# Optimization experiments

Measured on AMD Instinct MI355X. Metric: run time of the kernel, lower is better.

Reference implementation:

```python
import jax, jax.numpy as jnp
import numpy as np

B, N, NC = 16, 25200, 80          # batch, raw predictions, classes (COCO)
CONF_THRES = 0.25
IOU_THRES = 0.45
MAX_CAND = 1000                    # candidates kept after score top-k (pre-NMS)
CLS_OFFSET = 4096.0                # class-wise box offset (non-agnostic NMS trick)
EPS = 1e-7


def setup_inputs() -> dict:
    key = jax.random.key(0)
    # raw head output: [x, y, w, h, obj, cls0..cls79], values in [0,1]
    pred = jax.random.uniform(key, (B, N, 5 + NC), dtype=jnp.float32)
    return {"pred": pred}


def _xywh2xyxy(x):
    xy, wh = x[..., :2], x[..., 2:4]
    return jnp.concatenate([xy - wh * 0.5, xy + wh * 0.5], axis=-1)


def _box_iou(boxes):
    # boxes: [C, 4] xyxy -> pairwise IoU [C, C]
    area = (boxes[:, 2] - boxes[:, 0]) * (boxes[:, 3] - boxes[:, 1])
    lt = jnp.maximum(boxes[:, None, :2], boxes[None, :, :2])
    rb = jnp.minimum(boxes[:, None, 2:], boxes[None, :, 2:])
    wh = jnp.clip(rb - lt, 0.0)
    inter = wh[..., 0] * wh[..., 1]
    return inter / (area[:, None] + area[None, :] - inter + EPS)


def _nms_single(p):
    # p: [N, 5+NC] -> (out [MAX_CAND, 6] xyxy/conf/cls zero-padded, keep [MAX_CAND] bool)
    obj = p[:, 4]
    cls_scores = p[:, 5:] * obj[:, None]          # conf = obj * cls
    conf = jnp.max(cls_scores, axis=-1)
    cls_idx = jnp.argmax(cls_scores, axis=-1)
    valid = (obj > CONF_THRES) & (conf > CONF_THRES)
    score = jnp.where(valid, conf, -1.0)

    # pre-NMS top-k by score (sorted descending) — fixed-shape stand-in for boolean filter
    top_scores, idx = jax.lax.top_k(score, MAX_CAND)
    boxes = _xywh2xyxy(p[idx, :4])                # [C, 4]
    kconf = conf[idx]
    kcls = cls_idx[idx].astype(jnp.float32)
    valid_c = top_scores > 0.0

    # class-offset boxes so different classes never overlap (agnostic=False)
    off_boxes = boxes + kcls[:, None] * CLS_OFFSET
    iou = _box_iou(off_boxes)                     # [C, C]

    ar = jnp.arange(MAX_CAND)

    def body(i, keep):
        sup = keep[i] & (iou[i] > IOU_THRES) & (ar > i)
        return keep & jnp.logical_not(sup)

    keep = jax.lax.fori_loop(0, MAX_CAND, body, valid_c)

    out = jnp.concatenate([boxes, kconf[:, None], kcls[:, None]], axis=-1)  # [C, 6]
    out = jnp.where(keep[:, None], out, 0.0)
    return out, keep


def reference(pred):
    out, keep = jax.vmap(_nms_single)(pred)
    return out, keep
```

## Files before the change

### kernel.cpp

```cpp
#include <hip/hip_runtime.h>
#include <stdint.h>

typedef unsigned int u32;
typedef unsigned long long u64;

#define BATCH 16
#define NANCH 25200
#define NCLS 80
#define ROWF 85
#define MAXC 1000
#define CONF_T 0.25f
#define IOU_T 0.45f
#define EPS_F 1e-7f
#define APT (NANCH/4)

__device__ __forceinline__ float iou_ref(float4 a, float4 b) {
#pragma clang fp contract(off)
  float ai = (a.z - a.x) * (a.w - a.y);
  float aj = (b.z - b.x) * (b.w - b.y);
  float ltx = fmaxf(a.x, b.x), lty = fmaxf(a.y, b.y);
  float rbx = fminf(a.z, b.z), rby = fminf(a.w, b.w);
  float wx = fmaxf(rbx - ltx, 0.0f), wy = fmaxf(rby - lty, 0.0f);
  float inter = wx * wy;
  return inter / (ai + aj - inter + EPS_F);
}

__global__ __launch_bounds__(256) void k1_score(const float* __restrict__ pred,
                                                u64* __restrict__ keys,
                                                u32* __restrict__ hist) {
  __shared__ u32 lh[512];
  int tid = threadIdx.x;
  for (int i = tid; i < 512; i += 256) lh[i] = 0;
  __syncthreads();
  int t = blockIdx.x * 256 + tid;
  int b0 = (blockIdx.x * 256) / APT;
  if (t < BATCH * APT) {
    int b = t / APT;
    int n0 = (t % APT) * 4;
    const float4* src = (const float4*)(pred + ((size_t)b * NANCH + n0) * ROWF);
    float obj[4] = {0, 0, 0, 0};
    float best[4] = {-1e30f, -1e30f, -1e30f, -1e30f};
    int bidx[4] = {0, 0, 0, 0};
#pragma unroll
    for (int v = 0; v < ROWF; ++v) {
      float4 q = src[v];
      float vals[4] = {q.x, q.y, q.z, q.w};
#pragma unroll
      for (int k2 = 0; k2 < 4; ++k2) {
        const int e = 4 * v + k2;
        const int a = e / ROWF;
        const int f = e % ROWF;
        float val = vals[k2];
        if (f == 4) obj[a] = val;
        else if (f >= 5) {
          float s = val * obj[a];
          if (s > best[a]) { best[a] = s; bidx[a] = f - 5; }
        }
      }
    }
    int slot = b - b0;
#pragma unroll
    for (int a = 0; a < 4; ++a) {
      int n = n0 + a;
      float conf = best[a];
      bool valid = (obj[a] > CONF_T) && (conf > CONF_T);
      u32 hi;
      if (valid) hi = __float_as_uint(conf) | 0x80000000u;
      else hi = ((u32)n * 2654435761u) >> 1;
      u32 lo = ((u32)(32767 - n) << 7) | (u32)bidx[a];
      keys[(size_t)b * NANCH + n] = ((u64)hi << 32) | lo;
      atomicAdd(&lh[slot * 256 + (hi >> 24)], 1u);
    }
  }
  __syncthreads();
  for (int i = tid; i < 512; i += 256) {
    u32 v = lh[i];
    int bb = b0 + (i >> 8);
    if (v && bb < BATCH) atomicAdd(&hist[bb * 256 + (i & 255)], v);
  }
}

__global__ __launch_bounds__(1024) void k2_select(const float* __restrict__ pred,
                                                  const u64* __restrict__ keys,
                                                  const u32* __restrict__ hist,
                                                  float* __restrict__ selbox,
                                                  float* __restrict__ offbox,
                                                  float* __restrict__ selconf,
                                                  float* __restrict__ selcls,
                                                  u32* __restrict__ selvalid) {
  int b = blockIdx.x;
  int tid = threadIdx.x;
  __shared__ u32 h[256];
  __shared__ u32 sh_sel;
  __shared__ int sh_rank;
  __shared__ u32 scount;
  __shared__ u64 skey[2048];

  const u32* hik = (const u32*)(keys + (size_t)b * NANCH);
  u32 prefix = 0;
  for (int r = 0; r < 4; ++r) {
    if (r == 0) {
      if (tid < 256) h[tid] = hist[b * 256 + tid];
    } else {
      if (tid < 256) h[tid] = 0;
      __syncthreads();
      int shift = 24 - 8 * r;
      for (int i = tid; i < NANCH; i += 1024) {
        u32 hi = hik[2 * i + 1];
        if ((hi >> (shift + 8)) == prefix)
          atomicAdd(&h[(hi >> shift) & 255u], 1u);
      }
    }
    __syncthreads();
    if (tid < 64) {
      int l = tid;
      u32 a0 = h[4 * l + 0], a1 = h[4 * l + 1], a2 = h[4 * l + 2], a3 = h[4 * l + 3];
      u32 lane_sum = a0 + a1 + a2 + a3;
      u32 suf = lane_sum;
#pragma unroll
      for (int off = 1; off < 64; off <<= 1) {
        u32 tv = __shfl_down(suf, off);
        if (l + off < 64) suf += tv;
      }
      int rank = (r == 0) ? MAXC : sh_rank;
      u32 e3 = suf - lane_sum; u32 i3 = e3 + a3;
      u32 e2 = i3;             u32 i2 = e2 + a2;
      u32 e1 = i2;             u32 i1 = e1 + a1;
      u32 e0 = i1;             u32 i0 = e0 + a0;
      if ((int)i3 >= rank && (int)e3 < rank) { sh_sel = 4u * l + 3u; sh_rank = rank - (int)e3; }
      if ((int)i2 >= rank && (int)e2 < rank) { sh_sel = 4u * l + 2u; sh_rank = rank - (int)e2; }
      if ((int)i1 >= rank && (int)e1 < rank) { sh_sel = 4u * l + 1u; sh_rank = rank - (int)e1; }
      if ((int)i0 >= rank && (int)e0 < rank) { sh_sel = 4u * l + 0u; sh_rank = rank - (int)e0; }
    }
    __syncthreads();
    prefix = (r == 0) ? sh_sel : ((prefix << 8) | sh_sel);
  }
  u32 Cstar = prefix;

  if (tid == 0) scount = 0;
  skey[tid] = ~0ull;
  skey[tid + 1024] = ~0ull;
  __syncthreads();
  for (int i = tid; i < NANCH; i += 1024) {
    u64 k = keys[(size_t)b * NANCH + i];
    if ((u32)(k >> 32) >= Cstar) {
      u32 p = atomicAdd(&scount, 1u);
      if (p < 2048) skey[p] = ~k;
    }
  }
  __syncthreads();
  for (u32 kk = 2; kk <= 2048; kk <<= 1) {
    for (u32 j = kk >> 1; j > 0; j >>= 1) {
      for (int idx = tid; idx < 2048; idx += 1024) {
        u32 ixj = (u32)idx ^ j;
        if (ixj > (u32)idx) {
          u64 a = skey[idx], c2 = skey[ixj];
          bool up = ((idx & kk) == 0);
          if (up ? (a > c2) : (a < c2)) { skey[idx] = c2; skey[ixj] = a; }
        }
      }
      __syncthreads();
    }
  }
  if (tid < MAXC) {
    u64 k = ~skey[tid];
    u32 hi = (u32)(k >> 32);
    u32 lo = (u32)k;
    u32 n = 32767u - (lo >> 7);
    u32 ci = lo & 127u;
    bool valid = hi > 0x80000000u;
    float conf = valid ? __uint_as_float(hi & 0x7FFFFFFFu) : 0.0f;
    const float* pr = pred + ((size_t)b * NANCH + n) * ROWF;
    float x = pr[0], y = pr[1], w = pr[2], h2 = pr[3];
    float x1 = x - w * 0.5f, y1 = y - h2 * 0.5f;
    float x2 = x + w * 0.5f, y2 = y + h2 * 0.5f;
    float cf = (float)ci;
    float off = cf * 4096.0f;
    int o4 = (b * MAXC + tid) * 4;
    selbox[o4 + 0] = x1; selbox[o4 + 1] = y1; selbox[o4 + 2] = x2; selbox[o4 + 3] = y2;
    offbox[o4 + 0] = x1 + off; offbox[o4 + 1] = y1 + off;
    offbox[o4 + 2] = x2 + off; offbox[o4 + 3] = y2 + off;
    selconf[b * MAXC + tid] = conf;
    selcls[b * MAXC + tid] = cf;
    selvalid[b * MAXC + tid] = valid ? 1u : 0u;
  }
}

__global__ __launch_bounds__(256) void k3_dt(const float4* __restrict__ offbox4,
                                             u64* __restrict__ dt) {
  int wid = blockIdx.x * 4 + (threadIdx.x >> 6);
  int lane = threadIdx.x & 63;
  int b = wid / MAXC;
  int i = wid % MAXC;
  float4 bi = offbox4[b * MAXC + i];
  u64 myword = 0;
  for (int w = 0; w < 16; ++w) {
    int j = w * 64 + lane;
    int jc = (j < MAXC) ? j : 0;
    float4 bj = offbox4[b * MAXC + jc];
    float iou = iou_ref(bi, bj);
    bool bit = (iou > IOU_T) && (j < i);
    u64 bal = __ballot(bit ? 1 : 0);
    if (lane == w) myword = bal;
  }
  if (lane < 16) dt[((size_t)b * MAXC + i) * 16 + lane] = myword;
}

__global__ __launch_bounds__(1024) void k4_jacobi(const u64* __restrict__ dt,
                                                  const u32* __restrict__ selvalid,
                                                  const float* __restrict__ selbox,
                                                  const float* __restrict__ selconf,
                                                  const float* __restrict__ selcls,
                                                  float* __restrict__ out) {
  int b = blockIdx.x;
  int tid = threadIdx.x;
  int wv = tid >> 6, lane = tid & 63;
  __shared__ u64 keepv[16];
  __shared__ u32 changed;
  bool valid = false;
  u64 dtr[16];
  if (tid < MAXC) {
    valid = selvalid[b * MAXC + tid] != 0u;
#pragma unroll
    for (int w = 0; w < 16; ++w) dtr[w] = dt[((size_t)b * MAXC + tid) * 16 + w];
  } else {
#pragma unroll
    for (int w = 0; w < 16; ++w) dtr[w] = 0ull;
  }
  u64 bal0 = __ballot(valid ? 1 : 0);
  if (tid == 0) changed = 0;
  if (lane == 0) keepv[wv] = bal0;
  __syncthreads();
  for (int pass = 0; pass < MAXC; ++pass) {
    u64 kv[16];
#pragma unroll
    for (int w = 0; w < 16; ++w) kv[w] = keepv[w];
    u64 s = 0;
#pragma unroll
    for (int w = 0; w < 16; ++w) s |= dtr[w] & kv[w];
    bool nk = valid && (s == 0ull);
    u64 bal = __ballot(nk ? 1 : 0);
    __syncthreads();
    if (lane == 0 && bal != kv[wv]) { keepv[wv] = bal; atomicOr(&changed, 1u); }
    __syncthreads();
    u32 ch = changed;
    __syncthreads();
    if (tid == 0) changed = 0;
    if (!ch) break;
  }
  if (tid < MAXC) {
    bool kept = ((keepv[wv] >> lane) & 1ull) != 0ull;
    size_t o = (size_t)b * MAXC + tid;
    const float4* sb4 = (const float4*)selbox;
    float4 bx = sb4[o];
    float cf = selconf[o], cl = selcls[o];
    float* orow = out + o * 6;
    orow[0] = kept ? bx.x : 0.0f;
    orow[1] = kept ? bx.y : 0.0f;
    orow[2] = kept ? bx.z : 0.0f;
    orow[3] = kept ? bx.w : 0.0f;
    orow[4] = kept ? cf : 0.0f;
    orow[5] = kept ? cl : 0.0f;
    out[(size_t)BATCH * MAXC * 6 + o] = kept ? 1.0f : 0.0f;
  }
}

extern "C" void kernel_launch(void* const* d_in, const int* in_sizes, int n_in,
                              void* d_out, int out_size, void* d_ws, size_t ws_size,
                              hipStream_t stream) {
  const float* pred = (const float*)d_in[0];
  float* out = (float*)d_out;
  char* ws = (char*)d_ws;
  size_t off = 0;
  auto alloc = [&](size_t bytes) -> void* {
    void* p = ws + off;
    off = (off + bytes + 255) & ~(size_t)255;
    return p;
  };
  u64* keys     = (u64*)alloc((size_t)BATCH * NANCH * 8);
  u32* hist     = (u32*)alloc((size_t)BATCH * 256 * 4);
  float* selbox = (float*)alloc((size_t)BATCH * MAXC * 4 * 4);
  float* offbox = (float*)alloc((size_t)BATCH * MAXC * 4 * 4);
  float* selconf= (float*)alloc((size_t)BATCH * MAXC * 4);
  float* selcls = (float*)alloc((size_t)BATCH * MAXC * 4);
  u32* selvalid = (u32*)alloc((size_t)BATCH * MAXC * 4);
  u64* dt       = (u64*)alloc((size_t)BATCH * MAXC * 16 * 8);
  (void)ws_size; (void)in_sizes; (void)n_in; (void)out_size;

  hipMemsetAsync(hist, 0, (size_t)BATCH * 256 * 4, stream);

  int k1_blocks = (BATCH * APT + 255) / 256;
  k1_score<<<k1_blocks, 256, 0, stream>>>(pred, keys, hist);
  k2_select<<<BATCH, 1024, 0, stream>>>(pred, keys, hist, selbox, offbox,
                                        selconf, selcls, selvalid);
  k3_dt<<<(BATCH * MAXC) / 4, 256, 0, stream>>>((const float4*)offbox, dt);
  k4_jacobi<<<BATCH, 1024, 0, stream>>>(dt, selvalid, selbox, selconf,
                                        selcls, out);
}
```

Before: 280.6 us.

## Stage score rows through shared memory with coalesced loads and 4-way class split

```diff
diff --git a/kernel.cpp b/kernel.cpp
--- a/kernel.cpp
+++ b/kernel.cpp
@@ -12,7 +12,8 @@
 #define CONF_T 0.25f
 #define IOU_T 0.45f
 #define EPS_F 1e-7f
-#define APT (NANCH/4)
+#define TILE 64
+#define NTILES ((NANCH + TILE - 1) / TILE)
 
 __device__ __forceinline__ float iou_ref(float4 a, float4 b) {
 #pragma clang fp contract(off)
@@ -28,56 +29,60 @@
 __global__ __launch_bounds__(256) void k1_score(const float* __restrict__ pred,
                                                 u64* __restrict__ keys,
                                                 u32* __restrict__ hist) {
-  __shared__ u32 lh[512];
+  __shared__ float srow[TILE * ROWF];
+  __shared__ u64 skeys[TILE];
+  __shared__ u32 lh[256];
   int tid = threadIdx.x;
-  for (int i = tid; i < 512; i += 256) lh[i] = 0;
-  __syncthreads();
-  int t = blockIdx.x * 256 + tid;
-  int b0 = (blockIdx.x * 256) / APT;
-  if (t < BATCH * APT) {
-    int b = t / APT;
-    int n0 = (t % APT) * 4;
-    const float4* src = (const float4*)(pred + ((size_t)b * NANCH + n0) * ROWF);
-    float obj[4] = {0, 0, 0, 0};
-    float best[4] = {-1e30f, -1e30f, -1e30f, -1e30f};
-    int bidx[4] = {0, 0, 0, 0};
-#pragma unroll
-    for (int v = 0; v < ROWF; ++v) {
-      float4 q = src[v];
-      float vals[4] = {q.x, q.y, q.z, q.w};
-#pragma unroll
-      for (int k2 = 0; k2 < 4; ++k2) {
-        const int e = 4 * v + k2;
-        const int a = e / ROWF;
-        const int f = e % ROWF;
-        float val = vals[k2];
-        if (f == 4) obj[a] = val;
-        else if (f >= 5) {
-          float s = val * obj[a];
-          if (s > best[a]) { best[a] = s; bidx[a] = f - 5; }
-        }
-      }
-    }
-    int slot = b - b0;
-#pragma unroll
-    for (int a = 0; a < 4; ++a) {
-      int n = n0 + a;
-      float conf = best[a];
-      bool valid = (obj[a] > CONF_T) && (conf > CONF_T);
-      u32 hi;
-      if (valid) hi = __float_as_uint(conf) | 0x80000000u;
-      else hi = ((u32)n * 2654435761u) >> 1;
-      u32 lo = ((u32)(32767 - n) << 7) | (u32)bidx[a];
-      keys[(size_t)b * NANCH + n] = ((u64)hi << 32) | lo;
-      atomicAdd(&lh[slot * 256 + (hi >> 24)], 1u);
-    }
-  }
-  __syncthreads();
-  for (int i = tid; i < 512; i += 256) {
-    u32 v = lh[i];
-    int bb = b0 + (i >> 8);
-    if (v && bb < BATCH) atomicAdd(&hist[bb * 256 + (i & 255)], v);
-  }
+  int b = blockIdx.y;
+  int t0 = blockIdx.x * TILE;
+  int ntile = (t0 + TILE <= NANCH) ? TILE : (NANCH - t0);
+  int nf4 = (ntile * ROWF) >> 2;
+
+  lh[tid] = 0;
+  const float4* src4 = (const float4*)(pred + ((size_t)b * NANCH + t0) * ROWF);
+  float4* smem4 = (float4*)srow;
+#pragma unroll
+  for (int k = 0; k < 6; ++k) {
+    int i = k * 256 + tid;
+    if (i < nf4) smem4[i] = src4[i];
+  }
+  __syncthreads();
+
+  int a = tid >> 2;
+  int q = tid & 3;
+  float best = -1e30f;
+  int bidx = 0;
+  float obj = 0.0f;
+  if (a < ntile) {
+    const float* row = srow + a * ROWF;
+    obj = row[4];
+    int c0 = q * 20;
+#pragma unroll
+    for (int c = 0; c < 20; ++c) {
+      float s = row[5 + c0 + c] * obj;
+      if (s > best) { best = s; bidx = c0 + c; }
+    }
+  }
+#pragma unroll
+  for (int off = 1; off < 4; off <<= 1) {
+    float ob = __shfl_xor(best, off);
+    int oi = __shfl_xor(bidx, off);
+    if (ob > best || (ob == best && oi < bidx)) { best = ob; bidx = oi; }
+  }
+  if (q == 0 && a < ntile) {
+    int n = t0 + a;
+    bool valid = (obj > CONF_T) && (best > CONF_T);
+    u32 hi;
+    if (valid) hi = __float_as_uint(best) | 0x80000000u;
+    else hi = ((u32)n * 2654435761u) >> 1;
+    u32 lo = ((u32)(32767 - n) << 7) | (u32)bidx;
+    skeys[a] = ((u64)hi << 32) | lo;
+    atomicAdd(&lh[hi >> 24], 1u);
+  }
+  __syncthreads();
+  if (tid < ntile) keys[(size_t)b * NANCH + t0 + tid] = skeys[tid];
+  u32 v = lh[tid];
+  if (v) atomicAdd(&hist[b * 256 + tid], v);
 }
 
 __global__ __launch_bounds__(1024) void k2_select(const float* __restrict__ pred,
@@ -289,8 +294,8 @@
 
   hipMemsetAsync(hist, 0, (size_t)BATCH * 256 * 4, stream);
 
-  int k1_blocks = (BATCH * APT + 255) / 256;
-  k1_score<<<k1_blocks, 256, 0, stream>>>(pred, keys, hist);
+  dim3 g1(NTILES, BATCH);
+  k1_score<<<g1, 256, 0, stream>>>(pred, keys, hist);
   k2_select<<<BATCH, 1024, 0, stream>>>(pred, keys, hist, selbox, offbox,
                                         selconf, selcls, selvalid);
   k3_dt<<<(BATCH * MAXC) / 4, 256, 0, stream>>>((const float4*)offbox, dt);
```

After: 284.2 us. No clear change (+1.3%).
